# Optimization experiments

Measured on AMD Instinct MI355X. Metric: run time of the kernel, lower is better.

The kernel has to match this reference:

```python
import jax, jax.numpy as jnp
import numpy as np

L, D, H, HD, M = 4096, 1024, 16, 64, 4096
EPS = 1e-5


def setup_inputs() -> dict:
    key = jax.random.key(0)
    ks = jax.random.split(key, 12)
    hidden_states = jax.random.normal(ks[0], (L, D), dtype=jnp.float32)
    cu_seqlens = jnp.arange(5, dtype=jnp.int32) * (L // 4)  # [0,1024,2048,3072,4096]
    # rope freqs as cos/sin of random angles: (L, HD//2, 2)
    angles = jax.random.uniform(ks[1], (L, HD // 2), dtype=jnp.float32) * (2.0 * np.pi)
    rope_freqs = jnp.stack([jnp.cos(angles), jnp.sin(angles)], axis=-1)
    s = 0.02
    params = {
        "ln0_g": jnp.ones((D,), jnp.float32), "ln0_b": jnp.zeros((D,), jnp.float32),
        "ln1_g": jnp.ones((D,), jnp.float32), "ln1_b": jnp.zeros((D,), jnp.float32),
        "w_qkv": jax.random.normal(ks[2], (D, 3 * D), jnp.float32) * s,
        "w_o":   jax.random.normal(ks[3], (D, D), jnp.float32) * s,
        "w_fc0": jax.random.normal(ks[4], (D, M), jnp.float32) * s,
        "b_fc0": jnp.zeros((M,), jnp.float32),
        "w_fc1": jax.random.normal(ks[5], (M, D), jnp.float32) * s,
        "b_fc1": jnp.zeros((D,), jnp.float32),
    }
    return {"hidden_states": hidden_states, "cu_seqlens": cu_seqlens, "rope_freqs": rope_freqs, **params}


def _layernorm(x, g, b):
    mu = jnp.mean(x, axis=-1, keepdims=True)
    var = jnp.var(x, axis=-1, keepdims=True)
    return (x - mu) * jax.lax.rsqrt(var + EPS) * g + b


def _apply_rope(x, fc):
    # x: (L, H, HD); fc: (L, HD//2, 2) -> broadcast over heads
    xr = x.reshape(L, H, HD // 2, 2)
    a, b = xr[..., 0], xr[..., 1]
    c, s = fc[:, None, :, 0], fc[:, None, :, 1]
    out = jnp.stack([a * c - b * s, a * s + b * c], axis=-1)
    return out.reshape(L, H, HD)


def reference(hidden_states, cu_seqlens, rope_freqs, ln0_g, ln0_b, ln1_g, ln1_b,
              w_qkv, w_o, w_fc0, b_fc0, w_fc1, b_fc1):
    residual = hidden_states
    x = _layernorm(hidden_states, ln0_g, ln0_b)
    qkv = (x @ w_qkv).reshape(L, 3, H, HD)
    q, k, v = qkv[:, 0], qkv[:, 1], qkv[:, 2]
    q = _apply_rope(q, rope_freqs)
    k = _apply_rope(k, rope_freqs)
    # block-diagonal mask from cu_seqlens
    seg = jnp.searchsorted(cu_seqlens[1:], jnp.arange(L, dtype=cu_seqlens.dtype), side="right")
    mask = seg[:, None] == seg[None, :]  # (L, L)
    scale = 1.0 / np.sqrt(HD)
    scores = jnp.einsum("lhd,mhd->hlm", q, k) * scale
    scores = jnp.where(mask[None], scores, jnp.float32(-1e30))
    probs = jax.nn.softmax(scores, axis=-1)
    attn = jnp.einsum("hlm,mhd->lhd", probs, v).reshape(L, D)
    attn = attn @ w_o
    h = residual + attn
    y = _layernorm(h, ln1_g, ln1_b)
    y = jax.nn.gelu(y @ w_fc0 + b_fc0, approximate=False) @ w_fc1 + b_fc1
    return h + y
```

## Files before the change

kernel.cpp:

```cpp
#include <hip/hip_runtime.h>
#include <cstdint>
#include <cmath>

#define L_ 4096
#define D_ 1024
#define H_ 16
#define HD_ 64
#define M_ 4096

typedef __bf16 bf16_t;
typedef __attribute__((ext_vector_type(8))) __bf16 bf16x8;
typedef __attribute__((ext_vector_type(4))) __bf16 bf16x4;
typedef __attribute__((ext_vector_type(4))) float f32x4;

#define WAIT_VM0 0x0f70
#define WAIT_LGKM0 0xc07f

__device__ __forceinline__ f32x4 mfma16(bf16x8 a, bf16x8 b, f32x4 c) {
    return __builtin_amdgcn_mfma_f32_16x16x32_bf16(a, b, c, 0, 0, 0);
}

__device__ __forceinline__ void gload_lds16(const bf16_t* g, bf16_t* l) {
    __builtin_amdgcn_global_load_lds(
        (const __attribute__((address_space(1))) unsigned int*)(g),
        (__attribute__((address_space(3))) unsigned int*)(l), 16, 0, 0);
}

__device__ __forceinline__ float fast_exp2(float x) {
    float r;
    asm volatile("v_exp_f32 %0, %1" : "=v"(r) : "v"(x));
    return r;
}
__device__ __forceinline__ float fast_rcp(float x) {
    float r;
    asm volatile("v_rcp_f32 %0, %1" : "=v"(r) : "v"(x));
    return r;
}
__device__ __forceinline__ float gelu_f(float v) {
    float t = v * (0.7978845608f + 0.0356774081f * v * v);
    return v * fast_rcp(1.f + fast_exp2(-2.885390082f * t));
}

__global__ __launch_bounds__(256) void ln_kernel(const float* __restrict__ x,
                                                 const float* __restrict__ g,
                                                 const float* __restrict__ b,
                                                 bf16_t* __restrict__ out) {
    int row = blockIdx.x, tid = threadIdx.x;
    int wave = tid >> 6, lane = tid & 63;
    const f32x4* xr = (const f32x4*)(x + (long)row * D_);
    f32x4 v = xr[tid];
    float s = v.x + v.y + v.z + v.w;
    __shared__ float red[8];
#pragma unroll
    for (int off = 32; off > 0; off >>= 1) s += __shfl_down(s, off, 64);
    if (lane == 0) red[wave] = s;
    __syncthreads();
    float mean = (red[0] + red[1] + red[2] + red[3]) * (1.f / 1024.f);
    float s2 = 0.f;
#pragma unroll
    for (int i = 0; i < 4; i++) { float d = v[i] - mean; s2 += d * d; }
#pragma unroll
    for (int off = 32; off > 0; off >>= 1) s2 += __shfl_down(s2, off, 64);
    __syncthreads();
    if (lane == 0) red[wave] = s2;
    __syncthreads();
    float var = (red[0] + red[1] + red[2] + red[3]) * (1.f / 1024.f);
    float rstd = rsqrtf(var + 1e-5f);
    f32x4 g4 = ((const f32x4*)g)[tid];
    f32x4 b4 = ((const f32x4*)b)[tid];
    bf16x4 o;
#pragma unroll
    for (int i = 0; i < 4; i++) o[i] = (bf16_t)((v[i] - mean) * rstd * g4[i] + b4[i]);
    *(bf16x4*)(out + (long)row * D_ + tid * 4) = o;
}

__global__ __launch_bounds__(256) void transpose_all(
    const float* __restrict__ w_qkv, const float* __restrict__ w_o,
    const float* __restrict__ w_fc0, const float* __restrict__ w_fc1,
    bf16_t* __restrict__ t_qkv, bf16_t* __restrict__ t_o,
    bf16_t* __restrict__ t_fc0, bf16_t* __restrict__ t_fc1) {
    __shared__ float t[32][33];
    int bidx = blockIdx.x;
    const float* W;
    bf16_t* Wt;
    int K, N, tile;
    if (bidx < 3072) { W = w_qkv; Wt = t_qkv; K = 1024; N = 3072; tile = bidx; }
    else if (bidx < 4096) { W = w_o; Wt = t_o; K = 1024; N = 1024; tile = bidx - 3072; }
    else if (bidx < 8192) { W = w_fc0; Wt = t_fc0; K = 1024; N = 4096; tile = bidx - 4096; }
    else { W = w_fc1; Wt = t_fc1; K = 4096; N = 1024; tile = bidx - 8192; }
    int nt = N >> 5;
    int n0 = (tile % nt) * 32, k0 = (tile / nt) * 32;
    int tx = threadIdx.x & 31, ty = threadIdx.x >> 5;
#pragma unroll
    for (int r = 0; r < 32; r += 8)
        t[ty + r][tx] = W[(long)(k0 + ty + r) * N + n0 + tx];
    __syncthreads();
#pragma unroll
    for (int r = 0; r < 32; r += 8)
        Wt[(long)(n0 + ty + r) * K + k0 + tx] = (bf16_t)t[tx][ty + r];
}

__global__ __launch_bounds__(256) void vt_kernel(const bf16_t* __restrict__ qkv,
                                                 bf16_t* __restrict__ Vt) {
    __shared__ bf16_t t[32][33];
    int l0 = blockIdx.x * 32, c0 = blockIdx.y * 32;
    int tx = threadIdx.x & 31, ty = threadIdx.x >> 5;
#pragma unroll
    for (int r = 0; r < 32; r += 8)
        t[ty + r][tx] = qkv[(long)(l0 + ty + r) * 3072 + 2048 + c0 + tx];
    __syncthreads();
#pragma unroll
    for (int r = 0; r < 32; r += 8)
        Vt[(long)(c0 + ty + r) * 4096 + l0 + tx] = t[tx][ty + r];
}

__global__ __launch_bounds__(256) void rope_kernel(bf16_t* __restrict__ qkv,
                                                   const float* __restrict__ freqs) {
    const float k1 = 0.125f * 1.44269504089f;
    int idx = blockIdx.x * 256 + threadIdx.x;
    int g = idx & 7;
    int h = (idx >> 3) & 15;
    int l = idx >> 7;
    const float* f = freqs + (long)l * 64 + g * 8;
    f32x4 f0 = ((const f32x4*)f)[0];
    f32x4 f1 = ((const f32x4*)f)[1];
    float c[4] = {f0.x, f0.z, f1.x, f1.z};
    float s[4] = {f0.y, f0.w, f1.y, f1.w};
    bf16_t* qp = qkv + (long)l * 3072 + h * 64 + g * 8;
    bf16x8 q = *(bf16x8*)qp;
    bf16x8 k = *(bf16x8*)(qp + 1024);
    bf16x8 qo, ko;
#pragma unroll
    for (int e = 0; e < 4; e++) {
        float a = (float)q[2 * e], b = (float)q[2 * e + 1];
        qo[2 * e] = (bf16_t)((a * c[e] - b * s[e]) * k1);
        qo[2 * e + 1] = (bf16_t)((a * s[e] + b * c[e]) * k1);
        a = (float)k[2 * e]; b = (float)k[2 * e + 1];
        ko[2 * e] = (bf16_t)(a * c[e] - b * s[e]);
        ko[2 * e + 1] = (bf16_t)(a * s[e] + b * c[e]);
    }
    *(bf16x8*)qp = qo;
    *(bf16x8*)(qp + 1024) = ko;
}

template <int EPI, int GN, int SWBN, int SWBM>
__global__ __launch_bounds__(256) void gemm_bt(const bf16_t* __restrict__ A,
                                               const bf16_t* __restrict__ Bt,
                                               int M, int N, int K,
                                               bf16_t* __restrict__ outB,
                                               const float* __restrict__ bias) {
    __shared__ __align__(16) bf16_t As[128 * 64];
    __shared__ __align__(16) bf16_t Bs[128 * 64];
    int tid = threadIdx.x;
    int wave = tid >> 6, lane = tid & 63;
    int quad = lane >> 4, l16 = lane & 15;
    int wr = wave >> 1, wc = wave & 1;

    int g = blockIdx.x & 7, w = blockIdx.x >> 3;
    int gn_idx = g % GN, gm_idx = g / GN;
    int bn_i = gn_idx * SWBN + (w % SWBN);
    int bm_i = gm_idx * SWBM + (w / SWBN);
    long bm = (long)bm_i * 128, bn = (long)bn_i * 128;

    f32x4 acc[4][4];
#pragma unroll
    for (int i = 0; i < 4; i++)
#pragma unroll
        for (int j = 0; j < 4; j++) acc[i][j] = (f32x4){0.f, 0.f, 0.f, 0.f};

    int lr = lane >> 3;
    int sc = (lane & 7) ^ (lr & 7);
    const bf16_t* a_base = A + (bm + wave * 32 + lr) * (long)K + sc * 8;
    const bf16_t* b_base = Bt + (bn + wave * 32 + lr) * (long)K + sc * 8;

    for (int k0 = 0; k0 < K; k0 += 64) {
        __syncthreads();
#pragma unroll
        for (int i = 0; i < 4; i++) {
            gload_lds16(a_base + k0 + (long)(8 * i) * K, &As[(wave * 32 + 8 * i) * 64]);
            gload_lds16(b_base + k0 + (long)(8 * i) * K, &Bs[(wave * 32 + 8 * i) * 64]);
        }
        __builtin_amdgcn_s_waitcnt(WAIT_VM0);
        __syncthreads();

#pragma unroll
        for (int h = 0; h < 2; h++) {
            int sl = (h * 4 + quad) ^ (l16 & 7);
            bf16x8 af[4], bfr[4];
#pragma unroll
            for (int i = 0; i < 4; i++) {
                af[i] = *(const bf16x8*)&As[(wr * 64 + i * 16 + l16) * 64 + sl * 8];
                bfr[i] = *(const bf16x8*)&Bs[(wc * 64 + i * 16 + l16) * 64 + sl * 8];
            }
#pragma unroll
            for (int i = 0; i < 4; i++)
#pragma unroll
                for (int j = 0; j < 4; j++)
                    acc[i][j] = mfma16(af[i], bfr[j], acc[i][j]);
        }
    }

    long base_row = bm + wr * 64;
    long base_col = bn + wc * 64;
#pragma unroll
    for (int i = 0; i < 4; i++)
#pragma unroll
        for (int j = 0; j < 4; j++)
#pragma unroll
            for (int r = 0; r < 4; r++) {
                long row = base_row + i * 16 + quad * 4 + r;
                long col = base_col + j * 16 + l16;
                long idx = row * (long)N + col;
                float v = acc[i][j][r];
                if (EPI == 0) {
                    outB[idx] = (bf16_t)v;
                } else {
                    v += bias[col];
                    outB[idx] = (bf16_t)gelu_f(v);
                }
            }
}

__global__ __launch_bounds__(256) void gemm_splitk_store(const bf16_t* __restrict__ A,
                                                         const bf16_t* __restrict__ Bt,
                                                         int M, int N, int K, int Kc,
                                                         bf16_t* __restrict__ P) {
    __shared__ __align__(16) bf16_t As[128 * 64];
    __shared__ __align__(16) bf16_t Bs[128 * 64];
    int tid = threadIdx.x;
    int wave = tid >> 6, lane = tid & 63;
    int quad = lane >> 4, l16 = lane & 15;
    int wr = wave >> 1, wc = wave & 1;

    int g = blockIdx.x & 7, w = blockIdx.x >> 3;
    int z = g & 3, bm_hi = g >> 2;
    int bn_i = w & 7, bm_i = bm_hi * 16 + (w >> 3);
    long bm = (long)bm_i * 128, bn = (long)bn_i * 128;
    int kbeg = z * Kc, kend = kbeg + Kc;
    bf16_t* myP = P + (long)z * M * N;

    f32x4 acc[4][4];
#pragma unroll
    for (int i = 0; i < 4; i++)
#pragma unroll
        for (int j = 0; j < 4; j++) acc[i][j] = (f32x4){0.f, 0.f, 0.f, 0.f};

    int lr = lane >> 3;
    int sc = (lane & 7) ^ (lr & 7);
    const bf16_t* a_base = A + (bm + wave * 32 + lr) * (long)K + sc * 8;
    const bf16_t* b_base = Bt + (bn + wave * 32 + lr) * (long)K + sc * 8;

    for (int k0 = kbeg; k0 < kend; k0 += 64) {
        __syncthreads();
#pragma unroll
        for (int i = 0; i < 4; i++) {
            gload_lds16(a_base + k0 + (long)(8 * i) * K, &As[(wave * 32 + 8 * i) * 64]);
            gload_lds16(b_base + k0 + (long)(8 * i) * K, &Bs[(wave * 32 + 8 * i) * 64]);
        }
        __builtin_amdgcn_s_waitcnt(WAIT_VM0);
        __syncthreads();

#pragma unroll
        for (int h = 0; h < 2; h++) {
            int sl = (h * 4 + quad) ^ (l16 & 7);
            bf16x8 af[4], bfr[4];
#pragma unroll
            for (int i = 0; i < 4; i++) {
                af[i] = *(const bf16x8*)&As[(wr * 64 + i * 16 + l16) * 64 + sl * 8];
                bfr[i] = *(const bf16x8*)&Bs[(wc * 64 + i * 16 + l16) * 64 + sl * 8];
            }
#pragma unroll
            for (int i = 0; i < 4; i++)
#pragma unroll
                for (int j = 0; j < 4; j++)
                    acc[i][j] = mfma16(af[i], bfr[j], acc[i][j]);
        }
    }

    long base_row = bm + wr * 64;
    long base_col = bn + wc * 64;
#pragma unroll
    for (int i = 0; i < 4; i++)
#pragma unroll
        for (int j = 0; j < 4; j++)
#pragma unroll
            for (int r = 0; r < 4; r++) {
                long row = base_row + i * 16 + quad * 4 + r;
                long col = base_col + j * 16 + l16;
                myP[row * (long)N + col] = (bf16_t)acc[i][j][r];
            }
}

__global__ __launch_bounds__(256) void reduce_fc1(const bf16_t* __restrict__ P,
                                                  const float* __restrict__ bias,
                                                  float* __restrict__ out) {
    long i = (long)blockIdx.x * 256 + threadIdx.x;
    f32x4 b = ((const f32x4*)bias)[i & 255];
    f32x4 v = ((f32x4*)out)[i];
#pragma unroll
    for (int z = 0; z < 4; z++) {
        bf16x4 p = ((const bf16x4*)(P + (long)z * L_ * D_))[i];
#pragma unroll
        for (int e = 0; e < 4; e++) v[e] += (float)p[e];
    }
    v.x += b.x; v.y += b.y; v.z += b.z; v.w += b.w;
    ((f32x4*)out)[i] = v;
}

__global__ __launch_bounds__(256) void gemm_bt64_res(const bf16_t* __restrict__ A,
                                                     const bf16_t* __restrict__ Bt,
                                                     int M, int N, int K,
                                                     float* __restrict__ outF,
                                                     const float* __restrict__ res) {
    __shared__ __align__(16) bf16_t As[128 * 64];
    __shared__ __align__(16) bf16_t Bs[64 * 64];
    int tid = threadIdx.x;
    int wave = tid >> 6, lane = tid & 63;
    int quad = lane >> 4, l16 = lane & 15;

    int g = blockIdx.x & 7, w = blockIdx.x >> 3;
    int bn_i = w & 15, bm_i = g * 4 + (w >> 4);
    long bm = (long)bm_i * 128, bn = (long)bn_i * 64;

    f32x4 acc[2][4];
#pragma unroll
    for (int i = 0; i < 2; i++)
#pragma unroll
        for (int j = 0; j < 4; j++) acc[i][j] = (f32x4){0.f, 0.f, 0.f, 0.f};

    int lr = lane >> 3;
    int sc = (lane & 7) ^ (lr & 7);
    const bf16_t* a_base = A + (bm + wave * 32 + lr) * (long)K + sc * 8;
    const bf16_t* b_base = Bt + (bn + wave * 16 + lr) * (long)K + sc * 8;

    for (int k0 = 0; k0 < K; k0 += 64) {
        __syncthreads();
#pragma unroll
        for (int i = 0; i < 4; i++)
            gload_lds16(a_base + k0 + (long)(8 * i) * K, &As[(wave * 32 + 8 * i) * 64]);
#pragma unroll
        for (int i = 0; i < 2; i++)
            gload_lds16(b_base + k0 + (long)(8 * i) * K, &Bs[(wave * 16 + 8 * i) * 64]);
        __builtin_amdgcn_s_waitcnt(WAIT_VM0);
        __syncthreads();

#pragma unroll
        for (int h = 0; h < 2; h++) {
            int sl = (h * 4 + quad) ^ (l16 & 7);
            bf16x8 af[2], bfr[4];
#pragma unroll
            for (int i = 0; i < 2; i++)
                af[i] = *(const bf16x8*)&As[(wave * 32 + i * 16 + l16) * 64 + sl * 8];
#pragma unroll
            for (int j = 0; j < 4; j++)
                bfr[j] = *(const bf16x8*)&Bs[(j * 16 + l16) * 64 + sl * 8];
#pragma unroll
            for (int i = 0; i < 2; i++)
#pragma unroll
                for (int j = 0; j < 4; j++)
                    acc[i][j] = mfma16(af[i], bfr[j], acc[i][j]);
        }
    }

#pragma unroll
    for (int i = 0; i < 2; i++)
#pragma unroll
        for (int j = 0; j < 4; j++)
#pragma unroll
            for (int r = 0; r < 4; r++) {
                long row = bm + wave * 32 + i * 16 + quad * 4 + r;
                long col = bn + j * 16 + l16;
                long idx = row * (long)N + col;
                outF[idx] = acc[i][j][r] + res[idx];
            }
}

__global__ __launch_bounds__(256) void attn_kernel(const bf16_t* __restrict__ qkv,
                                                   const bf16_t* __restrict__ Vt,
                                                   const int* __restrict__ cu,
                                                   bf16_t* __restrict__ out) {
    __shared__ __align__(16) bf16_t QPs[4 * 16 * 72];
    __shared__ __align__(16) bf16_t Ks[2][64 * 64];
    __shared__ __align__(16) bf16_t Vs[2][64 * 64];

    int tid = threadIdx.x, wave = tid >> 6, lane = tid & 63;
    int quad = lane >> 4, l16 = lane & 15;

    int g = blockIdx.x & 7, w = blockIdx.x >> 3;
    int head = (w & 1) * 8 + g;
    int qt = (w >> 1) & 15;
    int seg = w >> 5;
    int s0 = cu[seg], s1 = cu[seg + 1];
    int r0 = s0 + qt * 64;
    const long hoff = (long)head * 64;

    bf16_t* Qs = QPs;
    bf16_t* Psw = &QPs[wave * 16 * 72];

    int lr = lane >> 3;
    int sc = (lane & 7) ^ (lr & 7);
    int sl0 = (0 * 4 + quad) ^ (l16 & 7);
    int sl1 = (1 * 4 + quad) ^ (l16 & 7);

#pragma unroll
    for (int i = 0; i < 2; i++) {
        int row = wave * 16 + i * 8 + lr;
        gload_lds16(qkv + (long)(r0 + row) * 3072 + hoff + sc * 8,
                    &Qs[(wave * 16 + i * 8) * 64]);
    }
    __builtin_amdgcn_s_waitcnt(WAIT_VM0);
    __syncthreads();
    bf16x8 aq0 = *(const bf16x8*)&Qs[(wave * 16 + l16) * 64 + sl0 * 8];
    bf16x8 aq1 = *(const bf16x8*)&Qs[(wave * 16 + l16) * 64 + sl1 * 8];

    bf16x8 ones;
#pragma unroll
    for (int e = 0; e < 8; e++) ones[e] = (bf16_t)1.0f;

    f32x4 o[4];
#pragma unroll
    for (int j = 0; j < 4; j++) o[j] = (f32x4){0.f, 0.f, 0.f, 0.f};
    f32x4 lacc = (f32x4){0.f, 0.f, 0.f, 0.f};

    for (int kt = s0; kt < s1; kt += 128) {
        __syncthreads();
#pragma unroll
        for (int i = 0; i < 2; i++) {
            int row = wave * 16 + i * 8 + lr;
            long kr0 = (long)(kt + row) * 3072 + 1024 + hoff + sc * 8;
            gload_lds16(qkv + kr0, &Ks[0][(wave * 16 + i * 8) * 64]);
            gload_lds16(qkv + kr0 + (long)64 * 3072, &Ks[1][(wave * 16 + i * 8) * 64]);
            long vr0 = (hoff + row) * (long)4096 + kt + sc * 8;
            gload_lds16(Vt + vr0, &Vs[0][(wave * 16 + i * 8) * 64]);
            gload_lds16(Vt + vr0 + 64, &Vs[1][(wave * 16 + i * 8) * 64]);
        }
        __builtin_amdgcn_s_waitcnt(WAIT_VM0);
        __syncthreads();

#pragma unroll
        for (int half = 0; half < 2; half++) {
            f32x4 sacc[4];
#pragma unroll
            for (int j = 0; j < 4; j++) sacc[j] = (f32x4){0.f, 0.f, 0.f, 0.f};
#pragma unroll
            for (int j = 0; j < 4; j++) {
                bf16x8 b0 = *(const bf16x8*)&Ks[half][(j * 16 + l16) * 64 + sl0 * 8];
                bf16x8 b1 = *(const bf16x8*)&Ks[half][(j * 16 + l16) * 64 + sl1 * 8];
                sacc[j] = mfma16(aq0, b0, sacc[j]);
                sacc[j] = mfma16(aq1, b1, sacc[j]);
            }

#pragma unroll
            for (int j = 0; j < 4; j++)
#pragma unroll
                for (int r = 0; r < 4; r++)
                    Psw[(quad * 4 + r) * 72 + j * 16 + l16] = (bf16_t)fast_exp2(sacc[j][r]);

            __builtin_amdgcn_s_waitcnt(WAIT_LGKM0);

            bf16x8 ap0 = *(const bf16x8*)&Psw[l16 * 72 + 0 * 32 + quad * 8];
            bf16x8 ap1 = *(const bf16x8*)&Psw[l16 * 72 + 1 * 32 + quad * 8];
#pragma unroll
            for (int j2 = 0; j2 < 4; j2++) {
                bf16x8 b0 = *(const bf16x8*)&Vs[half][(j2 * 16 + l16) * 64 + sl0 * 8];
                bf16x8 b1 = *(const bf16x8*)&Vs[half][(j2 * 16 + l16) * 64 + sl1 * 8];
                o[j2] = mfma16(ap0, b0, o[j2]);
                o[j2] = mfma16(ap1, b1, o[j2]);
            }
            lacc = mfma16(ap0, ones, lacc);
            lacc = mfma16(ap1, ones, lacc);
        }
    }

#pragma unroll
    for (int r = 0; r < 4; r++) {
        float inv = fast_rcp(lacc[r]);
        int row = r0 + wave * 16 + quad * 4 + r;
#pragma unroll
        for (int j2 = 0; j2 < 4; j2++)
            out[(long)row * 1024 + head * 64 + j2 * 16 + l16] = (bf16_t)(o[j2][r] * inv);
    }
}

extern "C" void kernel_launch(void* const* d_in, const int* in_sizes, int n_in,
                              void* d_out, int out_size, void* d_ws, size_t ws_size,
                              hipStream_t stream) {
    const float* hidden = (const float*)d_in[0];
    const int* cu = (const int*)d_in[1];
    const float* freqs = (const float*)d_in[2];
    const float* ln0_g = (const float*)d_in[3];
    const float* ln0_b = (const float*)d_in[4];
    const float* ln1_g = (const float*)d_in[5];
    const float* ln1_b = (const float*)d_in[6];
    const float* w_qkv = (const float*)d_in[7];
    const float* w_o = (const float*)d_in[8];
    const float* w_fc0 = (const float*)d_in[9];
    const float* b_fc0 = (const float*)d_in[10];
    const float* w_fc1 = (const float*)d_in[11];
    const float* b_fc1 = (const float*)d_in[12];
    float* out = (float*)d_out;

    char* ws = (char*)d_ws;
    bf16_t* qkv = (bf16_t*)(ws);
    bf16_t* attn = (bf16_t*)(ws + ((size_t)24 << 20));
    bf16_t* act = (bf16_t*)(ws);
    bf16_t* x_bf = (bf16_t*)(ws + ((size_t)32 << 20));
    bf16_t* Vt = x_bf;
    bf16_t* y_bf = x_bf;
    bf16_t* fc1p = (bf16_t*)(ws + ((size_t)40 << 20));
    bf16_t* wqkvT = (bf16_t*)(ws + ((size_t)72 << 20));
    bf16_t* woT = (bf16_t*)(ws + ((size_t)78 << 20));
    bf16_t* wfc0T = (bf16_t*)(ws + ((size_t)80 << 20));
    bf16_t* wfc1T = (bf16_t*)(ws + ((size_t)88 << 20));
    float* h = out;

    transpose_all<<<12288, 256, 0, stream>>>(w_qkv, w_o, w_fc0, w_fc1,
                                             wqkvT, woT, wfc0T, wfc1T);

    ln_kernel<<<L_, 256, 0, stream>>>(hidden, ln0_g, ln0_b, x_bf);

    gemm_bt<0, 2, 12, 8><<<768, 256, 0, stream>>>(
        x_bf, wqkvT, L_, 3072, 1024, qkv, nullptr);

    rope_kernel<<<(L_ * H_ * 8) / 256, 256, 0, stream>>>(qkv, freqs);
    vt_kernel<<<dim3(4096 / 32, 1024 / 32), 256, 0, stream>>>(qkv, Vt);

    attn_kernel<<<1024, 256, 0, stream>>>(qkv, Vt, cu, attn);

    gemm_bt64_res<<<512, 256, 0, stream>>>(
        attn, woT, L_, 1024, 1024, h, hidden);

    ln_kernel<<<L_, 256, 0, stream>>>(h, ln1_g, ln1_b, y_bf);

    gemm_bt<2, 4, 8, 16><<<1024, 256, 0, stream>>>(
        y_bf, wfc0T, L_, 4096, 1024, act, b_fc0);

    gemm_splitk_store<<<1024, 256, 0, stream>>>(
        act, wfc1T, L_, 1024, 4096, 1024, fc1p);
    reduce_fc1<<<(L_ * D_ / 4) / 256, 256, 0, stream>>>(fc1p, b_fc1, out);
}
```

Baseline: 337.1 us.

## Replace 128x128 GEMMs with double-buffered 256x256 8-wave ping-pong pipeline

Replaces the 128x128 single-buffered GEMM kernels for QKV, FC0 and split-K FC1 with a shared 256x256-tile core that runs 512 threads per block. The core double-buffers its LDS stages and interleaves async global-to-LDS loads with MFMA phases. It uses explicit barriers, priority boosts and vmcnt waits to overlap loads with compute. The larger tiles cut global traffic per FLOP, but they raise LDS and register use and launch only 192-256 blocks, so occupancy and tail balance could suffer.

```diff
diff --git a/kernel.cpp b/kernel.cpp
--- a/kernel.cpp
+++ b/kernel.cpp
@@ -143,75 +143,127 @@
     *(bf16x8*)(qp + 1024) = ko;
 }
 
-template <int EPI, int GN, int SWBN, int SWBM>
-__global__ __launch_bounds__(256) void gemm_bt(const bf16_t* __restrict__ A,
-                                               const bf16_t* __restrict__ Bt,
-                                               int M, int N, int K,
-                                               bf16_t* __restrict__ outB,
-                                               const float* __restrict__ bias) {
-    __shared__ __align__(16) bf16_t As[128 * 64];
-    __shared__ __align__(16) bf16_t Bs[128 * 64];
+#define PH_BAR1()                                        \
+    __builtin_amdgcn_sched_barrier(0);                   \
+    __builtin_amdgcn_s_barrier();                        \
+    asm volatile("s_waitcnt lgkmcnt(0)" ::: "memory");   \
+    __builtin_amdgcn_sched_barrier(0);                   \
+    __builtin_amdgcn_s_setprio(1);
+
+#define PH_BAR2()                                        \
+    __builtin_amdgcn_s_setprio(0);                       \
+    __builtin_amdgcn_sched_barrier(0);                   \
+    __builtin_amdgcn_s_barrier();                        \
+    __builtin_amdgcn_sched_barrier(0);
+
+#define STAGE_A(d, h, kt)                                                          \
+    gload_lds16(aSt + (long)((h) * 128) * K + (kt), &SA[d][h][(wv * 16) * 64]);    \
+    gload_lds16(aSt + (long)((h) * 128 + 8) * K + (kt), &SA[d][h][(wv * 16 + 8) * 64]);
+
+#define STAGE_B(d, h, kt)                                                          \
+    gload_lds16(bSt + (long)((h) * 128) * K + (kt), &SB[d][h][(wv * 16) * 64]);    \
+    gload_lds16(bSt + (long)((h) * 128 + 8) * K + (kt), &SB[d][h][(wv * 16 + 8) * 64]);
+
+#define RD_A(dst, src, rq)                                                          \
+    _Pragma("unroll") for (int i_ = 0; i_ < 4; i_++) {                              \
+        dst[i_][0] = *(const bf16x8*)&src[((rq) * 64 + i_ * 16 + l16) * 64 + sl0 * 8]; \
+        dst[i_][1] = *(const bf16x8*)&src[((rq) * 64 + i_ * 16 + l16) * 64 + sl1 * 8]; \
+    }
+
+#define RD_B(dst, src, cq)                                                          \
+    _Pragma("unroll") for (int j_ = 0; j_ < 2; j_++) {                              \
+        dst[j_][0] = *(const bf16x8*)&src[(bro + (cq) * 32 + j_ * 16 + l16) * 64 + sl0 * 8]; \
+        dst[j_][1] = *(const bf16x8*)&src[(bro + (cq) * 32 + j_ * 16 + l16) * 64 + sl1 * 8]; \
+    }
+
+#define MFMA_Q(rq, cq, Af, Bf)                                                      \
+    _Pragma("unroll") for (int i_ = 0; i_ < 4; i_++)                                \
+    _Pragma("unroll") for (int j_ = 0; j_ < 2; j_++) {                              \
+        acc[(rq) * 4 + i_][(cq) * 2 + j_] =                                         \
+            mfma16(Af[i_][0], Bf[j_][0], acc[(rq) * 4 + i_][(cq) * 2 + j_]);        \
+        acc[(rq) * 4 + i_][(cq) * 2 + j_] =                                         \
+            mfma16(Af[i_][1], Bf[j_][1], acc[(rq) * 4 + i_][(cq) * 2 + j_]);        \
+    }
+
+template <int EPI>
+__device__ __forceinline__ void gemm256_core(
+    const bf16_t* __restrict__ A, const bf16_t* __restrict__ Bt,
+    int K, int N, long bm, long bn, int kb, int ke,
+    bf16_t* __restrict__ outB, const float* __restrict__ bias) {
+    __shared__ __align__(16) bf16_t SA[2][2][128 * 64];
+    __shared__ __align__(16) bf16_t SB[2][2][128 * 64];
     int tid = threadIdx.x;
-    int wave = tid >> 6, lane = tid & 63;
+    int wv = tid >> 6, lane = tid & 63;
     int quad = lane >> 4, l16 = lane & 15;
-    int wr = wave >> 1, wc = wave & 1;
-
-    int g = blockIdx.x & 7, w = blockIdx.x >> 3;
-    int gn_idx = g % GN, gm_idx = g / GN;
-    int bn_i = gn_idx * SWBN + (w % SWBN);
-    int bm_i = gm_idx * SWBM + (w / SWBN);
-    long bm = (long)bm_i * 128, bn = (long)bn_i * 128;
-
-    f32x4 acc[4][4];
-#pragma unroll
-    for (int i = 0; i < 4; i++)
-#pragma unroll
-        for (int j = 0; j < 4; j++) acc[i][j] = (f32x4){0.f, 0.f, 0.f, 0.f};
-
+    int wm = wv >> 2, wn = wv & 3;
     int lr = lane >> 3;
     int sc = (lane & 7) ^ (lr & 7);
-    const bf16_t* a_base = A + (bm + wave * 32 + lr) * (long)K + sc * 8;
-    const bf16_t* b_base = Bt + (bn + wave * 32 + lr) * (long)K + sc * 8;
-
-    for (int k0 = 0; k0 < K; k0 += 64) {
-        __syncthreads();
-#pragma unroll
-        for (int i = 0; i < 4; i++) {
-            gload_lds16(a_base + k0 + (long)(8 * i) * K, &As[(wave * 32 + 8 * i) * 64]);
-            gload_lds16(b_base + k0 + (long)(8 * i) * K, &Bs[(wave * 32 + 8 * i) * 64]);
-        }
-        __builtin_amdgcn_s_waitcnt(WAIT_VM0);
-        __syncthreads();
-
-#pragma unroll
-        for (int h = 0; h < 2; h++) {
-            int sl = (h * 4 + quad) ^ (l16 & 7);
-            bf16x8 af[4], bfr[4];
-#pragma unroll
-            for (int i = 0; i < 4; i++) {
-                af[i] = *(const bf16x8*)&As[(wr * 64 + i * 16 + l16) * 64 + sl * 8];
-                bfr[i] = *(const bf16x8*)&Bs[(wc * 64 + i * 16 + l16) * 64 + sl * 8];
-            }
-#pragma unroll
-            for (int i = 0; i < 4; i++)
-#pragma unroll
-                for (int j = 0; j < 4; j++)
-                    acc[i][j] = mfma16(af[i], bfr[j], acc[i][j]);
-        }
-    }
-
-    long base_row = bm + wr * 64;
-    long base_col = bn + wc * 64;
-#pragma unroll
-    for (int i = 0; i < 4; i++)
-#pragma unroll
-        for (int j = 0; j < 4; j++)
+    int sl0 = quad ^ (l16 & 7);
+    int sl1 = (4 + quad) ^ (l16 & 7);
+    int bro = (wn & 1) * 64;
+
+    const bf16_t* aSt = A + (bm + wv * 16 + lr) * (long)K + sc * 8;
+    const bf16_t* bSt = Bt + (bn + wv * 16 + lr) * (long)K + sc * 8;
+    const bf16_t* pa0 = SA[0][wm];
+    const bf16_t* pa1 = SA[1][wm];
+    const bf16_t* pb0 = SB[0][wn >> 1];
+    const bf16_t* pb1 = SB[1][wn >> 1];
+
+    f32x4 acc[8][4];
+#pragma unroll
+    for (int i = 0; i < 8; i++)
+#pragma unroll
+        for (int j = 0; j < 4; j++) acc[i][j] = (f32x4){0.f, 0.f, 0.f, 0.f};
+
+    bf16x8 a0[4][2], a1[4][2], b0[2][2], b1[2][2];
+
+    STAGE_B(0, 0, kb); STAGE_A(0, 0, kb); STAGE_B(0, 1, kb); STAGE_A(0, 1, kb);
+    STAGE_B(1, 0, kb + 64); STAGE_A(1, 0, kb + 64); STAGE_B(1, 1, kb + 64);
+    asm volatile("s_waitcnt vmcnt(6)" ::: "memory");
+    __builtin_amdgcn_sched_barrier(0);
+    __builtin_amdgcn_s_barrier();
+    RD_B(b0, pb0, 0);
+
+    for (int k0 = kb; k0 < ke; k0 += 128) {
+        int kt2 = (k0 + 128 < ke) ? k0 + 128 : kb;
+        int kt3 = kt2 + 64;
+        RD_A(a0, pa0, 0); RD_B(b1, pb0, 1);
+        STAGE_A(1, 1, k0 + 64);
+        PH_BAR1(); MFMA_Q(0, 0, a0, b0); PH_BAR2();
+        RD_A(a1, pa0, 1);
+        STAGE_B(0, 0, kt2);
+        PH_BAR1(); MFMA_Q(0, 1, a0, b1); PH_BAR2();
+        STAGE_A(0, 0, kt2);
+        asm volatile("s_waitcnt vmcnt(4)" ::: "memory");
+        PH_BAR1(); MFMA_Q(1, 0, a1, b0); PH_BAR2();
+        RD_B(b0, pb1, 0);
+        STAGE_B(0, 1, kt2);
+        PH_BAR1(); MFMA_Q(1, 1, a1, b1); PH_BAR2();
+        RD_A(a0, pa1, 0); RD_B(b1, pb1, 1);
+        STAGE_A(0, 1, kt2);
+        PH_BAR1(); MFMA_Q(0, 0, a0, b0); PH_BAR2();
+        RD_A(a1, pa1, 1);
+        STAGE_B(1, 0, kt3);
+        PH_BAR1(); MFMA_Q(0, 1, a0, b1); PH_BAR2();
+        STAGE_A(1, 0, kt3);
+        asm volatile("s_waitcnt vmcnt(4)" ::: "memory");
+        PH_BAR1(); MFMA_Q(1, 0, a1, b0); PH_BAR2();
+        RD_B(b0, pb0, 0);
+        STAGE_B(1, 1, kt3);
+        PH_BAR1(); MFMA_Q(1, 1, a1, b1); PH_BAR2();
+    }
+    asm volatile("s_waitcnt vmcnt(0)" ::: "memory");
+
+#pragma unroll
+    for (int ri = 0; ri < 8; ri++)
+#pragma unroll
+        for (int cj = 0; cj < 4; cj++)
 #pragma unroll
             for (int r = 0; r < 4; r++) {
-                long row = base_row + i * 16 + quad * 4 + r;
-                long col = base_col + j * 16 + l16;
+                long row = bm + wm * 128 + (ri >> 2) * 64 + (ri & 3) * 16 + quad * 4 + r;
+                long col = bn + wn * 64 + (cj >> 1) * 32 + (cj & 1) * 16 + l16;
                 long idx = row * (long)N + col;
-                float v = acc[i][j][r];
+                float v = acc[ri][cj][r];
                 if (EPI == 0) {
                     outB[idx] = (bf16_t)v;
                 } else {
@@ -221,74 +273,36 @@
             }
 }
 
-__global__ __launch_bounds__(256) void gemm_splitk_store(const bf16_t* __restrict__ A,
-                                                         const bf16_t* __restrict__ Bt,
-                                                         int M, int N, int K, int Kc,
-                                                         bf16_t* __restrict__ P) {
-    __shared__ __align__(16) bf16_t As[128 * 64];
-    __shared__ __align__(16) bf16_t Bs[128 * 64];
-    int tid = threadIdx.x;
-    int wave = tid >> 6, lane = tid & 63;
-    int quad = lane >> 4, l16 = lane & 15;
-    int wr = wave >> 1, wc = wave & 1;
-
+__global__ __launch_bounds__(512) void gemm256_qkv(const bf16_t* __restrict__ A,
+                                                   const bf16_t* __restrict__ Bt,
+                                                   bf16_t* __restrict__ outB) {
     int g = blockIdx.x & 7, w = blockIdx.x >> 3;
-    int z = g & 3, bm_hi = g >> 2;
-    int bn_i = w & 7, bm_i = bm_hi * 16 + (w >> 3);
-    long bm = (long)bm_i * 128, bn = (long)bn_i * 128;
-    int kbeg = z * Kc, kend = kbeg + Kc;
-    bf16_t* myP = P + (long)z * M * N;
-
-    f32x4 acc[4][4];
-#pragma unroll
-    for (int i = 0; i < 4; i++)
-#pragma unroll
-        for (int j = 0; j < 4; j++) acc[i][j] = (f32x4){0.f, 0.f, 0.f, 0.f};
-
-    int lr = lane >> 3;
-    int sc = (lane & 7) ^ (lr & 7);
-    const bf16_t* a_base = A + (bm + wave * 32 + lr) * (long)K + sc * 8;
-    const bf16_t* b_base = Bt + (bn + wave * 32 + lr) * (long)K + sc * 8;
-
-    for (int k0 = kbeg; k0 < kend; k0 += 64) {
-        __syncthreads();
-#pragma unroll
-        for (int i = 0; i < 4; i++) {
-            gload_lds16(a_base + k0 + (long)(8 * i) * K, &As[(wave * 32 + 8 * i) * 64]);
-            gload_lds16(b_base + k0 + (long)(8 * i) * K, &Bs[(wave * 32 + 8 * i) * 64]);
-        }
-        __builtin_amdgcn_s_waitcnt(WAIT_VM0);
-        __syncthreads();
-
-#pragma unroll
-        for (int h = 0; h < 2; h++) {
-            int sl = (h * 4 + quad) ^ (l16 & 7);
-            bf16x8 af[4], bfr[4];
-#pragma unroll
-            for (int i = 0; i < 4; i++) {
-                af[i] = *(const bf16x8*)&As[(wr * 64 + i * 16 + l16) * 64 + sl * 8];
-                bfr[i] = *(const bf16x8*)&Bs[(wc * 64 + i * 16 + l16) * 64 + sl * 8];
-            }
-#pragma unroll
-            for (int i = 0; i < 4; i++)
-#pragma unroll
-                for (int j = 0; j < 4; j++)
-                    acc[i][j] = mfma16(af[i], bfr[j], acc[i][j]);
-        }
-    }
-
-    long base_row = bm + wr * 64;
-    long base_col = bn + wc * 64;
-#pragma unroll
-    for (int i = 0; i < 4; i++)
-#pragma unroll
-        for (int j = 0; j < 4; j++)
-#pragma unroll
-            for (int r = 0; r < 4; r++) {
-                long row = base_row + i * 16 + quad * 4 + r;
-                long col = base_col + j * 16 + l16;
-                myP[row * (long)N + col] = (bf16_t)acc[i][j][r];
-            }
+    int gm = g >> 2, gn = g & 3;
+    long bm = (long)(gm * 8 + w / 3) * 256;
+    long bn = (long)(gn * 3 + w % 3) * 256;
+    gemm256_core<0>(A, Bt, 1024, 3072, bm, bn, 0, 1024, outB, nullptr);
+}
+
+__global__ __launch_bounds__(512) void gemm256_fc0(const bf16_t* __restrict__ A,
+                                                   const bf16_t* __restrict__ Bt,
+                                                   bf16_t* __restrict__ outB,
+                                                   const float* __restrict__ bias) {
+    int g = blockIdx.x & 7, w = blockIdx.x >> 3;
+    int gm = g >> 2, gn = g & 3;
+    long bm = (long)(gm * 8 + (w >> 2)) * 256;
+    long bn = (long)(gn * 4 + (w & 3)) * 256;
+    gemm256_core<2>(A, Bt, 1024, 4096, bm, bn, 0, 1024, outB, bias);
+}
+
+__global__ __launch_bounds__(512) void gemm256_fc1(const bf16_t* __restrict__ A,
+                                                   const bf16_t* __restrict__ Bt,
+                                                   bf16_t* __restrict__ P) {
+    int g = blockIdx.x & 7, w = blockIdx.x >> 3;
+    int z = g >> 1, gm = g & 1;
+    long bm = (long)(gm * 8 + (w >> 2)) * 256;
+    long bn = (long)(w & 3) * 256;
+    gemm256_core<0>(A, Bt, 4096, 1024, bm, bn, z * 1024, z * 1024 + 1024,
+                    P + (long)z * L_ * D_, nullptr);
 }
 
 __global__ __launch_bounds__(256) void reduce_fc1(const bf16_t* __restrict__ P,
@@ -519,8 +533,7 @@
 
     ln_kernel<<<L_, 256, 0, stream>>>(hidden, ln0_g, ln0_b, x_bf);
 
-    gemm_bt<0, 2, 12, 8><<<768, 256, 0, stream>>>(
-        x_bf, wqkvT, L_, 3072, 1024, qkv, nullptr);
+    gemm256_qkv<<<192, 512, 0, stream>>>(x_bf, wqkvT, qkv);
 
     rope_kernel<<<(L_ * H_ * 8) / 256, 256, 0, stream>>>(qkv, freqs);
     vt_kernel<<<dim3(4096 / 32, 1024 / 32), 256, 0, stream>>>(qkv, Vt);
@@ -532,10 +545,8 @@
 
     ln_kernel<<<L_, 256, 0, stream>>>(h, ln1_g, ln1_b, y_bf);
 
-    gemm_bt<2, 4, 8, 16><<<1024, 256, 0, stream>>>(
-        y_bf, wfc0T, L_, 4096, 1024, act, b_fc0);
-
-    gemm_splitk_store<<<1024, 256, 0, stream>>>(
-        act, wfc1T, L_, 1024, 4096, 1024, fc1p);
+    gemm256_fc0<<<256, 512, 0, stream>>>(y_bf, wfc0T, act, b_fc0);
+
+    gemm256_fc1<<<256, 512, 0, stream>>>(act, wfc1T, fc1p);
     reduce_fc1<<<(L_ * D_ / 4) / 256, 256, 0, stream>>>(fc1p, b_fc1, out);
 }
```

Result: faster. 329.7 us (-2.2%).
